# Kernel tuning notes

Hardware: AMD Instinct MI355X
Metric: run time of the kernel (lower is better)

## Reference

```python
import jax, jax.numpy as jnp
import numpy as np

K = 4  # top-k from init
BN_IS_FOLDED = True  # BatchNorm (eval mode) folded into per-channel scale s and shift t


def tconv(x, W):
    # x: (b, C, v, n); W: (Cout, Cin, 3) temporal conv, kernel (3,1,1), padding (1,0,0), no bias
    return jax.lax.conv_general_dilated(
        x, W[:, :, :, None], window_strides=(1, 1),
        padding=((1, 1), (0, 0)), dimension_numbers=('NCHW', 'OIHW', 'NCHW'))


def gcn_single(xn, src, dst, Wg, bg):
    # PyG GCNConv: add self-loops, symmetric normalization, then scatter-add.
    N = xn.shape[0]
    xl = xn @ Wg  # (N, C)
    loop = jnp.arange(N, dtype=src.dtype)
    s = jnp.concatenate([src, loop])
    d = jnp.concatenate([dst, loop])
    deg = jax.ops.segment_sum(jnp.ones(s.shape[0], dtype=xn.dtype), d, num_segments=N)
    dinv = jnp.where(deg > 0, jax.lax.rsqrt(deg), 0.0)
    norm = dinv[s] * dinv[d]
    out = jax.ops.segment_sum(norm[:, None] * xl[s], d, num_segments=N)
    return out + bg


def setup_inputs() -> dict:
    key = jax.random.key(0)
    ks = jax.random.split(key, 10)
    C = 256
    x = jax.random.normal(ks[0], (512, C, 16, 16), dtype=jnp.float32)
    Wd = jax.random.normal(ks[1], (C, C, 3), dtype=jnp.float32) * 0.02
    s1 = 1.0 + 0.1 * jax.random.normal(ks[2], (C,), dtype=jnp.float32)
    t1 = 0.1 * jax.random.normal(ks[3], (C,), dtype=jnp.float32)
    Wg = jax.random.normal(ks[4], (C, C), dtype=jnp.float32) * 0.02
    bg = 0.01 * jax.random.normal(ks[5], (C,), dtype=jnp.float32)
    Wu = jax.random.normal(ks[6], (C, C, 3), dtype=jnp.float32) * 0.02
    s2 = 1.0 + 0.1 * jax.random.normal(ks[7], (C,), dtype=jnp.float32)
    t2 = 0.1 * jax.random.normal(ks[8], (C,), dtype=jnp.float32)
    return {"x": x, "batch": 4, "Wd": Wd, "s1": s1, "t1": t1,
            "Wg": Wg, "bg": bg, "Wu": Wu, "s2": s2, "t2": t2}


def reference(x, batch, Wd, s1, t1, Wg, bg, Wu, s2, t2):
    tlen, c, h, w = x.shape
    b = batch
    v = tlen // b
    hw = h * w
    # (tlen,c,h,w) -> (b,c,v,h*w)
    x4 = x.reshape(b, v, c, h, w).transpose(0, 2, 1, 3, 4).reshape(b, c, v, hw)
    xd = tconv(x4, Wd) * s1[None, :, None, None] + t1[None, :, None, None]  # down_conv + BN(eval)

    # --- dynamic graph build (no-grad in original) ---
    f = jax.lax.stop_gradient(xd).transpose(0, 2, 3, 1)  # (b, v, hw, c)
    f1, f2 = f[:, :-1], f[:, 1:]                          # (b, t_1, hw, c)
    t_1 = v - 1
    sq1 = jnp.sum(f1 * f1, axis=-1)                       # (b,t_1,hw)
    sq2 = jnp.sum(f2 * f2, axis=-1)
    dots = jnp.einsum('btnc,btmc->btnm', f1, f2)
    d2 = jnp.maximum(sq1[..., :, None] + sq2[..., None, :] - 2.0 * dots, 0.0)
    sim = -jnp.sqrt(d2).reshape(b, t_1, hw * hw)
    sim = sim / jnp.maximum(jnp.linalg.norm(sim, axis=-1, keepdims=True), 1e-12)  # F.normalize
    sim = jnp.where(sim < 0.05, 100.0, sim)
    _, idx = jax.lax.top_k(sim, K)                        # (b, t_1, K)
    frame = jnp.arange(t_1, dtype=jnp.int32)[None, :, None]
    row = (idx // hw).astype(jnp.int32) + frame * hw
    col = (idx % hw).astype(jnp.int32) + (frame + 1) * hw
    row = row.reshape(b, -1)
    col = col.reshape(b, -1)
    src = jnp.concatenate([row, col], axis=1)             # forward + reversed edges
    dst = jnp.concatenate([col, row], axis=1)

    # --- per-sample GCN (batched with vmap) ---
    nodes = xd.transpose(0, 2, 3, 1).reshape(b, v * hw, c)  # 'b c v n -> b (v n) c'
    out = jax.vmap(lambda xn, s, d: gcn_single(xn, s, d, Wg, bg))(nodes, src, dst)

    # --- up path ---
    o4 = out.transpose(0, 2, 1).reshape(b, c, v, hw)
    xu = tconv(o4, Wu) * s2[None, :, None, None] + t2[None, :, None, None]
    return xu.reshape(b, c, v, h, w).transpose(0, 2, 1, 3, 4).reshape(tlen, c, h, w)
```

## Files before the change

kernel.cpp:

```cpp
#include <hip/hip_runtime.h>

typedef __attribute__((ext_vector_type(8))) short short8;
typedef __attribute__((ext_vector_type(4))) float f32x4;
typedef unsigned short u16;
typedef unsigned int u32;

__device__ __forceinline__ void gld_lds16(const void* g, void* l) {
  __builtin_amdgcn_global_load_lds((const __attribute__((address_space(1))) void*)g,
                                   (__attribute__((address_space(3))) void*)l,
                                   16, 0, 0);
}

__device__ __forceinline__ u16 f2b(float x) {
  union { float f; u32 u; } v; v.f = x;
  u32 u = v.u;
  return (u16)((u + 0x7FFFu + ((u >> 16) & 1u)) >> 16);
}
__device__ __forceinline__ float b2f(u16 x) {
  union { u32 u; float f; } v; v.u = ((u32)x) << 16; return v.f;
}
__device__ __forceinline__ u32 pack_pair(float lo, float hi) {
  return (u32)f2b(lo) | ((u32)f2b(hi) << 16);
}

__global__ __launch_bounds__(256) void k_prep(const float* __restrict__ Wd, const float* __restrict__ Wg,
                                              const float* __restrict__ Wu,
                                              const float* __restrict__ s1, const float* __restrict__ t1,
                                              const float* __restrict__ bg,
                                              u16* __restrict__ WdT, u16* __restrict__ Wup,
                                              u16* __restrict__ WgS,
                                              float* __restrict__ c0, float* __restrict__ tWg) {
  int blk = blockIdx.x;
  int tid = threadIdx.x;
  if (blk == 1024) {
    int j = tid;
    float a = 0.f;
    for (int co = 0; co < 256; ++co) a += t1[co] * Wg[co * 256 + j];
    tWg[j] = a;
    c0[j] = a + bg[j];
    return;
  }
  int id = blk * 256 + tid;
  if (id < 196608) {
    int kk = id >> 16;
    int rem = id & 65535;
    int a = rem >> 8, b = rem & 255;
    Wup[id] = f2b(Wu[(u32)a * 768 + (u32)b * 3 + kk]);
    WdT[id] = f2b(Wd[(u32)b * 768 + (u32)a * 3 + kk]);
  } else {
    int id2 = id - 196608;
    int j = id2 >> 8, co = id2 & 255;
    WgS[id2] = f2b(Wg[co * 256 + j] * s1[co]);
  }
}

__global__ __launch_bounds__(256) void k_transpose(const float* __restrict__ x, u16* __restrict__ xT) {
  __shared__ u16 tile[64][72];
  int blk = blockIdx.x;
  int tl = blk >> 4;
  int sub = blk & 15;
  int ci0 = (sub >> 2) << 6;
  int p0 = (sub & 3) << 6;
  int tid = threadIdx.x;
  int i = tid >> 2;
  int ch = tid & 3;
  const float* gsrc = x + (size_t)tl * 65536 + (ci0 + i) * 256 + p0 + ch * 16;
  __align__(16) u16 cv[16];
#pragma unroll
  for (int v4 = 0; v4 < 4; ++v4) {
    float4 f = *(const float4*)(gsrc + v4 * 4);
    cv[v4 * 4 + 0] = f2b(f.x);
    cv[v4 * 4 + 1] = f2b(f.y);
    cv[v4 * 4 + 2] = f2b(f.z);
    cv[v4 * 4 + 3] = f2b(f.w);
  }
  *(uint4*)&tile[i][ch * 16] = *(const uint4*)&cv[0];
  *(uint4*)&tile[i][ch * 16 + 8] = *(const uint4*)&cv[8];
  __syncthreads();
  __align__(16) u16 tmp[16];
#pragma unroll
  for (int cc = 0; cc < 16; ++cc) tmp[cc] = tile[ch * 16 + cc][i];
  u16* gdst = xT + (size_t)tl * 65536 + (p0 + i) * 256 + ci0 + ch * 16;
  *(uint4*)(gdst) = *(const uint4*)&tmp[0];
  *(uint4*)(gdst + 8) = *(const uint4*)&tmp[8];
}

__device__ __forceinline__ void stage_tile(const u16* __restrict__ g, int ldg, u16* s, int w, int lane) {
  int r = lane >> 2;
  int cc = (lane & 3) * 8;
#pragma unroll
  for (int j = 0; j < 2; ++j) {
    gld_lds16(g + (w * 32 + j * 16 + r) * ldg + cc, s + (w * 32 + j * 16) * 32);
  }
}

__device__ __forceinline__ void mfma_tiles(const u16* sA, const u16* sB, f32x4 acc[4][4],
                                           int wr, int wc, int lane) {
  int m16 = lane & 15;
  int q8 = (lane >> 4) * 8;
  short8 a[4], b[4];
#pragma unroll
  for (int mi = 0; mi < 4; ++mi) a[mi] = *(const short8*)(sA + (wr * 64 + mi * 16 + m16) * 32 + q8);
#pragma unroll
  for (int ni = 0; ni < 4; ++ni) b[ni] = *(const short8*)(sB + (wc * 64 + ni * 16 + m16) * 32 + q8);
#pragma unroll
  for (int mi = 0; mi < 4; ++mi)
#pragma unroll
    for (int ni = 0; ni < 4; ++ni)
      acc[mi][ni] = __builtin_amdgcn_mfma_f32_16x16x32_bf16(a[mi], b[ni], acc[mi][ni], 0, 0, 0);
}

__device__ __forceinline__ void store_pairs(u16* base, int row0, int stride, int colb,
                                            const float v[4], bool ev) {
  float pv[4];
#pragma unroll
  for (int r = 0; r < 4; ++r) pv[r] = __shfl_xor(v[r], 1, 64);
  u32 wd0 = ev ? pack_pair(v[0], pv[0]) : pack_pair(pv[0], v[0]);
  u32 wd1 = ev ? pack_pair(v[1], pv[1]) : pack_pair(pv[1], v[1]);
  u32 wd2 = ev ? pack_pair(v[2], pv[2]) : pack_pair(pv[2], v[2]);
  u32 wd3 = ev ? pack_pair(v[3], pv[3]) : pack_pair(pv[3], v[3]);
  u32 wa = ev ? wd0 : wd2;
  u32 wb = ev ? wd1 : wd3;
  int rs = ev ? 0 : 2;
  *(u32*)(base + (size_t)(row0 + rs) * stride + colb) = wa;
  *(u32*)(base + (size_t)(row0 + rs + 1) * stride + colb) = wb;
}

__device__ __forceinline__ void store_pairs_f32(float* base, int row0, int stride, int colb,
                                                const float v[4], bool ev) {
  float pv[4];
#pragma unroll
  for (int r = 0; r < 4; ++r) pv[r] = __shfl_xor(v[r], 1, 64);
  float2 wa, wb;
  if (ev) { wa = make_float2(v[0], pv[0]); wb = make_float2(v[1], pv[1]); }
  else    { wa = make_float2(pv[2], v[2]); wb = make_float2(pv[3], v[3]); }
  int rs = ev ? 0 : 2;
  *(float2*)(base + (size_t)(row0 + rs) * stride + colb) = wa;
  *(float2*)(base + (size_t)(row0 + rs + 1) * stride + colb) = wb;
}

__global__ __launch_bounds__(256) void k_wcomb(const u16* __restrict__ WgS, const u16* __restrict__ WdT,
                                               u16* __restrict__ Wcomb) {
  __shared__ u16 sA[128 * 32];
  __shared__ u16 sB[128 * 32];
  int blk = blockIdx.x;
  int kk = blk >> 2;
  int tile = blk & 3;
  int tm = tile >> 1, tn = tile & 1;
  int tid = threadIdx.x, lane = tid & 63, w = tid >> 6;
  int wr = w >> 1, wc = w & 1;
  f32x4 acc[4][4];
#pragma unroll
  for (int i = 0; i < 4; ++i)
#pragma unroll
    for (int j = 0; j < 4; ++j) acc[i][j] = (f32x4){0.f, 0.f, 0.f, 0.f};
  const u16* gA = WgS + (size_t)(tm * 128) * 256;
  const u16* gB = WdT + (size_t)kk * 65536 + (size_t)(tn * 128) * 256;
  for (int ks = 0; ks < 8; ++ks) {
    stage_tile(gA + ks * 32, 256, sA, w, lane);
    stage_tile(gB + ks * 32, 256, sB, w, lane);
    __syncthreads();
    mfma_tiles(sA, sB, acc, wr, wc, lane);
    __syncthreads();
  }
  int q = lane >> 4, c = lane & 15;
  bool ev = (lane & 1) == 0;
  u16* obase = Wcomb + (size_t)kk * 65536;
#pragma unroll
  for (int mi = 0; mi < 4; ++mi) {
    int row0 = tm * 128 + wr * 64 + mi * 16 + q * 4;
#pragma unroll
    for (int ni = 0; ni < 4; ++ni) {
      float v[4];
#pragma unroll
      for (int r = 0; r < 4; ++r) v[r] = acc[mi][ni][r];
      int colb = tn * 128 + wc * 64 + ni * 16 + (c & ~1);
      store_pairs(obase, row0, 256, colb, v, ev);
    }
  }
}

__global__ __launch_bounds__(256) void k_g12(const u16* __restrict__ xT, const u16* __restrict__ Wcomb,
                                             const float* __restrict__ c0, const float* __restrict__ tWg,
                                             u16* __restrict__ outp, float* __restrict__ edge) {
  __shared__ u16 sA[2][128 * 32];
  __shared__ u16 sB[2][128 * 32];
  int b = blockIdx.x;
  int logical = (b & 7) * 256 + (b >> 3);
  int bt = logical >> 2;
  int tile = logical & 3;
  int tm = tile >> 1, tn = tile & 1;
  int t = bt & 127;
  int tid = threadIdx.x, lane = tid & 63, w = tid >> 6;
  int wr = w >> 1, wc = w & 1;
  f32x4 acc[4][4];
#pragma unroll
  for (int i = 0; i < 4; ++i)
#pragma unroll
    for (int j = 0; j < 4; ++j) acc[i][j] = (f32x4){0.f, 0.f, 0.f, 0.f};

  const u16* Ap[3];
  const u16* Bp[3];
  int nf = 0;
#pragma unroll
  for (int kk = 0; kk < 3; ++kk) {
    int tp = t - 1 + kk;
    if (tp < 0 || tp > 127) continue;
    Ap[nf] = xT + ((size_t)(bt - t + tp) * 256 + tm * 128) * 256;
    Bp[nf] = Wcomb + (size_t)kk * 65536 + (size_t)(tn * 128) * 256;
    ++nf;
  }
  int nc = nf * 8;
  stage_tile(Ap[0], 256, sA[0], w, lane);
  stage_tile(Bp[0], 256, sB[0], w, lane);
  __syncthreads();
  for (int c = 0; c < nc; ++c) {
    int nx = c + 1;
    if (nx < nc) {
      stage_tile(Ap[nx >> 3] + (nx & 7) * 32, 256, sA[nx & 1], w, lane);
      stage_tile(Bp[nx >> 3] + (nx & 7) * 32, 256, sB[nx & 1], w, lane);
    }
    mfma_tiles(sA[c & 1], sB[c & 1], acc, wr, wc, lane);
    __syncthreads();
  }

  int q = lane >> 4, cc16 = lane & 15;
  bool ev = (lane & 1) == 0;
  float c0v[4], tWgv[4];
#pragma unroll
  for (int ni = 0; ni < 4; ++ni) {
    int j = tn * 128 + wc * 64 + ni * 16 + cc16;
    c0v[ni] = c0[j];
    tWgv[ni] = tWg[j];
  }
  bool eblk = (tm == 0) && (wr == 0) && (q == 0);
  u16* obase = outp + (size_t)bt * 65536;
#pragma unroll
  for (int mi = 0; mi < 4; ++mi) {
    int row0 = tm * 128 + wr * 64 + mi * 16 + q * 4;
#pragma unroll
    for (int ni = 0; ni < 4; ++ni) {
      float v[4];
#pragma unroll
      for (int r = 0; r < 4; ++r) v[r] = acc[mi][ni][r] + c0v[ni];
      int colb = tn * 128 + wc * 64 + ni * 16 + (cc16 & ~1);
      store_pairs(obase, row0, 256, colb, v, ev);
      if (eblk && mi == 0) {
        float vE[4];
#pragma unroll
        for (int r = 0; r < 4; ++r) vE[r] = acc[0][ni][r] + tWgv[ni];
        store_pairs_f32(edge + (size_t)bt * 1024, 0, 256, colb, vE, ev);
      }
    }
  }
}

__device__ __forceinline__ float dinv0(int t) {
  if (t == 0) return 0.44721359549995793f;
  if (t == 127) return 0.7071067811865476f;
  return 0.4082482904638631f;
}
__global__ __launch_bounds__(256) void k_fix(const float* __restrict__ edge, const float* __restrict__ bg,
                                             u16* __restrict__ outp) {
  int bt = blockIdx.x;
  int t = bt & 127;
  int j = threadIdx.x;
  const float ISQ2 = 0.7071067811865476f;
  float bgv = bg[j];
  float e_t = edge[(size_t)bt * 1024 + j];
  float At = dinv0(t);
  float o0 = bgv + At * At * e_t;
  if (t <= 126) {
    float At1 = dinv0(t + 1);
    const float* en = edge + (size_t)(bt + 1) * 1024;
    float s = At1 * en[j] + ISQ2 * (en[256 + j] + en[512 + j] + en[768 + j]);
    o0 += At * s;
  }
  float em1 = 0.f, Atm1 = 0.f;
  if (t >= 1) {
    Atm1 = dinv0(t - 1);
    em1 = edge[(size_t)(bt - 1) * 1024 + j];
    o0 += At * Atm1 * em1;
  }
  u16* ob = outp + (size_t)bt * 65536;
  ob[j] = f2b(o0);
#pragma unroll
  for (int k = 1; k <= 3; ++k) {
    float m = edge[(size_t)bt * 1024 + k * 256 + j];
    float ok = (t == 0) ? (bgv + m) : (bgv + 0.5f * m + ISQ2 * Atm1 * em1);
    ob[k * 256 + j] = f2b(ok);
  }
}

__global__ __launch_bounds__(256) void k_g3(const u16* __restrict__ outp, const u16* __restrict__ Wup,
                                            const float* __restrict__ s2, const float* __restrict__ t2,
                                            float* __restrict__ y) {
  __shared__ u16 sA[2][128 * 32];
  __shared__ u16 sB[2][128 * 32];
  __shared__ float ss2[128], st2[128];
  int b = blockIdx.x;
  int logical = (b & 7) * 256 + (b >> 3);
  int bt = logical >> 2;
  int tile = logical & 3;
  int tm = tile >> 1, tn = tile & 1;
  int t = bt & 127;
  int tid = threadIdx.x, lane = tid & 63, w = tid >> 6;
  int wr = w >> 1, wc = w & 1;
  if (tid < 128) {
    int co = tm * 128 + tid;
    ss2[tid] = s2[co];
    st2[tid] = t2[co];
  }
  f32x4 acc[4][4];
#pragma unroll
  for (int i = 0; i < 4; ++i)
#pragma unroll
    for (int j = 0; j < 4; ++j) acc[i][j] = (f32x4){0.f, 0.f, 0.f, 0.f};

  const u16* Ap[3];
  const u16* Bp[3];
  int nf = 0;
#pragma unroll
  for (int kk = 0; kk < 3; ++kk) {
    int tp = t - 1 + kk;
    if (tp < 0 || tp > 127) continue;
    Ap[nf] = Wup + (size_t)kk * 65536 + (size_t)(tm * 128) * 256;
    Bp[nf] = outp + ((size_t)(bt - t + tp) * 256 + tn * 128) * 256;
    ++nf;
  }
  int nc = nf * 8;
  stage_tile(Ap[0], 256, sA[0], w, lane);
  stage_tile(Bp[0], 256, sB[0], w, lane);
  __syncthreads();
  for (int c = 0; c < nc; ++c) {
    int nx = c + 1;
    if (nx < nc) {
      stage_tile(Ap[nx >> 3] + (nx & 7) * 32, 256, sA[nx & 1], w, lane);
      stage_tile(Bp[nx >> 3] + (nx & 7) * 32, 256, sB[nx & 1], w, lane);
    }
    mfma_tiles(sA[c & 1], sB[c & 1], acc, wr, wc, lane);
    __syncthreads();
  }

  int q = lane >> 4, cc16 = lane & 15;
  bool ev = (lane & 1) == 0;
  float* ybase = y + (size_t)bt * 65536;
#pragma unroll
  for (int mi = 0; mi < 4; ++mi) {
    int rl = wr * 64 + mi * 16 + q * 4;
    float sv[4], tv[4];
#pragma unroll
    for (int r = 0; r < 4; ++r) { sv[r] = ss2[rl + r]; tv[r] = st2[rl + r]; }
#pragma unroll
    for (int ni = 0; ni < 4; ++ni) {
      float v[4];
#pragma unroll
      for (int r = 0; r < 4; ++r) v[r] = acc[mi][ni][r] * sv[r] + tv[r];
      int colb = tn * 128 + wc * 64 + ni * 16 + (cc16 & ~1);
      store_pairs_f32(ybase, tm * 128 + rl, 256, colb, v, ev);
    }
  }
}

extern "C" void kernel_launch(void* const* d_in, const int* in_sizes, int n_in,
                              void* d_out, int out_size, void* d_ws, size_t ws_size,
                              hipStream_t stream) {
  (void)in_sizes; (void)n_in; (void)out_size; (void)ws_size;
  const float* x  = (const float*)d_in[0];
  const float* Wd = (const float*)d_in[2];
  const float* s1 = (const float*)d_in[3];
  const float* t1 = (const float*)d_in[4];
  const float* Wg = (const float*)d_in[5];
  const float* bg = (const float*)d_in[6];
  const float* Wu = (const float*)d_in[7];
  const float* s2 = (const float*)d_in[8];
  const float* t2 = (const float*)d_in[9];
  float* y = (float*)d_out;
  char* ws = (char*)d_ws;
  u16*   outp  = (u16*)(ws);
  u16*   xT    = (u16*)(ws + 67108864);
  float* edge  = (float*)(ws + 134217728);
  u16*   WdT   = (u16*)(ws + 134217728);
  u16*   WgS   = (u16*)(ws + 134611072);
  u16*   Wup   = (u16*)(ws + 136314880);
  u16*   Wcomb = (u16*)(ws + 136708096);
  float* c0    = (float*)(ws + 137101312);
  float* tWg   = (float*)(ws + 137102336);

  k_prep<<<dim3(1025), dim3(256), 0, stream>>>(Wd, Wg, Wu, s1, t1, bg, WdT, Wup, WgS, c0, tWg);
  k_wcomb<<<dim3(12), dim3(256), 0, stream>>>(WgS, WdT, Wcomb);
  k_transpose<<<dim3(8192), dim3(256), 0, stream>>>(x, xT);
  k_g12<<<dim3(2048), dim3(256), 0, stream>>>(xT, Wcomb, c0, tWg, outp, edge);
  k_fix<<<dim3(512), dim3(256), 0, stream>>>(edge, bg, outp);
  k_g3<<<dim3(2048), dim3(256), 0, stream>>>(outp, Wup, s2, t2, y);
}
```

Baseline: 431.1 us.

## Use 256x256 tiles with zero-padded frames and 8-wave pipelined MFMA GEMM core

Restructures both GEMM kernels to have each 512-thread block compute a full 256x256 output tile per frame. Boundary frames are zero-padded on either side, so the three temporal taps always make a uniform K=768 loop with no branching. The new core uses XOR-swizzled LDS layout, finer-grained staging interleaved with MFMA quads, s_setprio and explicit vmcnt waits. The edge buffer is moved into the output array as scratch. This trades extra zeroing work and MFMA on padded zero frames for larger data reuse and better overlap of loads with compute.

```diff
diff --git a/kernel.cpp b/kernel.cpp
--- a/kernel.cpp
+++ b/kernel.cpp
@@ -4,6 +4,8 @@
 typedef __attribute__((ext_vector_type(4))) float f32x4;
 typedef unsigned short u16;
 typedef unsigned int u32;
+
+#define FENCE() asm volatile("" ::: "memory")
 
 __device__ __forceinline__ void gld_lds16(const void* g, void* l) {
   __builtin_amdgcn_global_load_lds((const __attribute__((address_space(1))) void*)g,
@@ -54,7 +56,18 @@
   }
 }
 
-__global__ __launch_bounds__(256) void k_transpose(const float* __restrict__ x, u16* __restrict__ xT) {
+__global__ __launch_bounds__(256) void k_zero(u16* __restrict__ outz, u16* __restrict__ xTz) {
+  int gid = blockIdx.x * 256 + threadIdx.x;
+  int i = gid * 8;
+  int buf = (i >= 327680) ? 1 : 0;
+  int wi = i - buf * 327680;
+  int f = wi >> 16;
+  int off = wi & 65535;
+  u16* dst = (buf ? xTz : outz) + (size_t)f * 129 * 65536 + off;
+  *(uint4*)dst = make_uint4(0u, 0u, 0u, 0u);
+}
+
+__global__ __launch_bounds__(256) void k_transpose(const float* __restrict__ x, u16* __restrict__ xTz) {
   __shared__ u16 tile[64][72];
   int blk = blockIdx.x;
   int tl = blk >> 4;
@@ -80,7 +93,8 @@
   __align__(16) u16 tmp[16];
 #pragma unroll
   for (int cc = 0; cc < 16; ++cc) tmp[cc] = tile[ch * 16 + cc][i];
-  u16* gdst = xT + (size_t)tl * 65536 + (p0 + i) * 256 + ci0 + ch * 16;
+  int fi = (tl >> 7) * 129 + (tl & 127) + 1;
+  u16* gdst = xTz + (size_t)fi * 65536 + (p0 + i) * 256 + ci0 + ch * 16;
   *(uint4*)(gdst) = *(const uint4*)&tmp[0];
   *(uint4*)(gdst + 8) = *(const uint4*)&tmp[8];
 }
@@ -180,77 +194,176 @@
   }
 }
 
-__global__ __launch_bounds__(256) void k_g12(const u16* __restrict__ xT, const u16* __restrict__ Wcomb,
-                                             const float* __restrict__ c0, const float* __restrict__ tWg,
-                                             u16* __restrict__ outp, float* __restrict__ edge) {
-  __shared__ u16 sA[2][128 * 32];
-  __shared__ u16 sB[2][128 * 32];
-  int b = blockIdx.x;
-  int logical = (b & 7) * 256 + (b >> 3);
-  int bt = logical >> 2;
-  int tile = logical & 3;
-  int tm = tile >> 1, tn = tile & 1;
-  int t = bt & 127;
-  int tid = threadIdx.x, lane = tid & 63, w = tid >> 6;
-  int wr = w >> 1, wc = w & 1;
-  f32x4 acc[4][4];
-#pragma unroll
-  for (int i = 0; i < 4; ++i)
+
+__device__ __forceinline__ void stage_part(int s, const u16* Ab, const u16* Bb,
+                                           u16* sA, u16* sB, int wuni, int g0) {
+  if (s >= 48) return;
+  const int tau = s >> 2;
+  const int pt = s & 3;
+  const int toff = ((tau >> 2) << 16) + ((tau & 3) << 6);
+  const int half = pt & 1;
+  const u16* src = ((pt & 2) ? Ab : Bb) + toff + (half << 15) + g0;
+  u16* dst = ((pt & 2) ? sA : sB) + ((tau & 1) << 14) + (half << 13) + wuni;
+  gld_lds16(src, dst);
+  gld_lds16(src + 16384, dst + 4096);
+}
+
+template<int QUAD, int NH>
+__device__ __forceinline__ void mfma_quad(f32x4 (&acc)[8][4], const short8 (&af)[2][4],
+                                          const short8 (&bf)[2][2][2]) {
+#pragma unroll
+  for (int k = 0; k < 2; ++k)
+#pragma unroll
+    for (int m = 0; m < 4; ++m)
+#pragma unroll
+      for (int nj = 0; nj < 2; ++nj)
+        acc[QUAD * 4 + m][NH * 2 + nj] = __builtin_amdgcn_mfma_f32_16x16x32_bf16(
+            af[k][m], bf[NH][k][nj], acc[QUAD * 4 + m][NH * 2 + nj], 0, 0, 0);
+}
+
+__device__ __forceinline__ void gemm256_core(const u16* __restrict__ Ab, const u16* __restrict__ Bb,
+                                             u16* sA, u16* sB, int tid, f32x4 (&acc)[8][4]) {
+  const int lane = tid & 63;
+  const int w = tid >> 6;
+  const int wr = w >> 2;
+  const int wc = w & 3;
+  const int m16 = lane & 15;
+  const int xorm = (lane & 7) << 4;
+  const int q16b = (lane >> 4) << 4;
+  const int koffe0 = ((q16b) ^ xorm) >> 1;
+  const int koffe1 = ((64 + q16b) ^ xorm) >> 1;
+  const int srow = tid >> 3;
+  const int scol = ((tid & 7) ^ (srow & 7)) << 3;
+  const int g0 = srow * 256 + scol;
+  const int wuni = w << 9;
+
+#pragma unroll
+  for (int i = 0; i < 8; ++i)
 #pragma unroll
     for (int j = 0; j < 4; ++j) acc[i][j] = (f32x4){0.f, 0.f, 0.f, 0.f};
 
-  const u16* Ap[3];
-  const u16* Bp[3];
-  int nf = 0;
-#pragma unroll
-  for (int kk = 0; kk < 3; ++kk) {
-    int tp = t - 1 + kk;
-    if (tp < 0 || tp > 127) continue;
-    Ap[nf] = xT + ((size_t)(bt - t + tp) * 256 + tm * 128) * 256;
-    Bp[nf] = Wcomb + (size_t)kk * 65536 + (size_t)(tn * 128) * 256;
-    ++nf;
-  }
-  int nc = nf * 8;
-  stage_tile(Ap[0], 256, sA[0], w, lane);
-  stage_tile(Bp[0], 256, sB[0], w, lane);
-  __syncthreads();
-  for (int c = 0; c < nc; ++c) {
-    int nx = c + 1;
-    if (nx < nc) {
-      stage_tile(Ap[nx >> 3] + (nx & 7) * 32, 256, sA[nx & 1], w, lane);
-      stage_tile(Bp[nx >> 3] + (nx & 7) * 32, 256, sB[nx & 1], w, lane);
-    }
-    mfma_tiles(sA[c & 1], sB[c & 1], acc, wr, wc, lane);
-    __syncthreads();
-  }
-
+#pragma unroll
+  for (int s = 0; s < 7; ++s) stage_part(s, Ab, Bb, sA, sB, wuni, g0);
+  asm volatile("s_waitcnt vmcnt(6)" ::: "memory");
+  __builtin_amdgcn_s_barrier();
+  FENCE();
+
+  short8 af[2][4];
+  short8 bf[2][2][2];
+#pragma unroll 2
+  for (int kt = 0; kt < 12; ++kt) {
+    const int cb = kt & 1;
+    const u16* aH = sA + cb * 16384 + wr * 8192;
+    const u16* bH = sB + cb * 16384 + (wc >> 1) * 8192;
+    const int bR0 = (wc & 1) << 6;
+#pragma unroll
+    for (int m = 0; m < 4; ++m) {
+      const u16* p = aH + (m * 16 + m16) * 64;
+      af[0][m] = *(const short8*)(p + koffe0);
+      af[1][m] = *(const short8*)(p + koffe1);
+    }
+#pragma unroll
+    for (int nh = 0; nh < 2; ++nh)
+#pragma unroll
+      for (int nj = 0; nj < 2; ++nj) {
+        const u16* p = bH + (bR0 + (nh * 2 + nj) * 16 + m16) * 64;
+        bf[nh][0][nj] = *(const short8*)(p + koffe0);
+        bf[nh][1][nj] = *(const short8*)(p + koffe1);
+      }
+    stage_part(4 * kt + 7, Ab, Bb, sA, sB, wuni, g0);
+    FENCE();
+    __builtin_amdgcn_s_barrier();
+    FENCE();
+    __builtin_amdgcn_s_setprio(1);
+    mfma_quad<0, 0>(acc, af, bf);
+    __builtin_amdgcn_s_setprio(0);
+    FENCE();
+    __builtin_amdgcn_s_barrier();
+    FENCE();
+    stage_part(4 * kt + 8, Ab, Bb, sA, sB, wuni, g0);
+    FENCE();
+    __builtin_amdgcn_s_barrier();
+    FENCE();
+    __builtin_amdgcn_s_setprio(1);
+    mfma_quad<0, 1>(acc, af, bf);
+    __builtin_amdgcn_s_setprio(0);
+    FENCE();
+    __builtin_amdgcn_s_barrier();
+    FENCE();
+#pragma unroll
+    for (int m = 0; m < 4; ++m) {
+      const u16* p = aH + (64 + m * 16 + m16) * 64;
+      af[0][m] = *(const short8*)(p + koffe0);
+      af[1][m] = *(const short8*)(p + koffe1);
+    }
+    stage_part(4 * kt + 9, Ab, Bb, sA, sB, wuni, g0);
+    FENCE();
+    __builtin_amdgcn_s_barrier();
+    FENCE();
+    __builtin_amdgcn_s_setprio(1);
+    mfma_quad<1, 0>(acc, af, bf);
+    __builtin_amdgcn_s_setprio(0);
+    FENCE();
+    __builtin_amdgcn_s_barrier();
+    FENCE();
+    stage_part(4 * kt + 10, Ab, Bb, sA, sB, wuni, g0);
+    FENCE();
+    __builtin_amdgcn_s_barrier();
+    FENCE();
+    __builtin_amdgcn_s_setprio(1);
+    mfma_quad<1, 1>(acc, af, bf);
+    __builtin_amdgcn_s_setprio(0);
+    if (kt < 10) asm volatile("s_waitcnt vmcnt(6)" ::: "memory");
+    else         asm volatile("s_waitcnt vmcnt(0)" ::: "memory");
+    __builtin_amdgcn_s_barrier();
+    FENCE();
+  }
+}
+
+__global__ __launch_bounds__(512, 2) void k_g12(const u16* __restrict__ xTz, const u16* __restrict__ Wcomb,
+                                                const float* __restrict__ c0, const float* __restrict__ tWg,
+                                                u16* __restrict__ outz, float* __restrict__ edge) {
+  __shared__ u16 sA[32768];
+  __shared__ u16 sB[32768];
+  int bsw = (int)blockIdx.x;
+  int bt = (bsw & 7) * 64 + (bsw >> 3);
+  int b = bt >> 7, t = bt & 127;
+  int tid = threadIdx.x;
+  const u16* Ab = xTz + (size_t)(b * 129 + t) * 65536;
+  const u16* Bb = Wcomb;
+  f32x4 acc[8][4];
+  gemm256_core(Ab, Bb, sA, sB, tid, acc);
+
+  int lane = tid & 63, w = tid >> 6, wr = w >> 2, wc = w & 3;
   int q = lane >> 4, cc16 = lane & 15;
   bool ev = (lane & 1) == 0;
   float c0v[4], tWgv[4];
 #pragma unroll
   for (int ni = 0; ni < 4; ++ni) {
-    int j = tn * 128 + wc * 64 + ni * 16 + cc16;
+    int j = wc * 64 + ni * 16 + cc16;
     c0v[ni] = c0[j];
     tWgv[ni] = tWg[j];
   }
-  bool eblk = (tm == 0) && (wr == 0) && (q == 0);
-  u16* obase = outp + (size_t)bt * 65536;
-#pragma unroll
-  for (int mi = 0; mi < 4; ++mi) {
-    int row0 = tm * 128 + wr * 64 + mi * 16 + q * 4;
+  u16* obase = outz + (size_t)(b * 129 + t + 1) * 65536;
+#pragma unroll
+  for (int mi = 0; mi < 8; ++mi) {
+    int row0 = wr * 128 + mi * 16 + q * 4;
 #pragma unroll
     for (int ni = 0; ni < 4; ++ni) {
       float v[4];
 #pragma unroll
       for (int r = 0; r < 4; ++r) v[r] = acc[mi][ni][r] + c0v[ni];
-      int colb = tn * 128 + wc * 64 + ni * 16 + (cc16 & ~1);
-      store_pairs(obase, row0, 256, colb, v, ev);
-      if (eblk && mi == 0) {
-        float vE[4];
-#pragma unroll
-        for (int r = 0; r < 4; ++r) vE[r] = acc[0][ni][r] + tWgv[ni];
-        store_pairs_f32(edge + (size_t)bt * 1024, 0, 256, colb, vE, ev);
-      }
+      store_pairs(obase, row0, 256, wc * 64 + ni * 16 + (cc16 & ~1), v, ev);
+    }
+  }
+  if (wr == 0 && q == 0) {
+    float* eb = edge + (size_t)bt * 1024;
+#pragma unroll
+    for (int ni = 0; ni < 4; ++ni) {
+      float vE[4];
+#pragma unroll
+      for (int r = 0; r < 4; ++r) vE[r] = acc[0][ni][r] + tWgv[ni];
+      store_pairs_f32(eb, 0, 256, wc * 64 + ni * 16 + (cc16 & ~1), vE, ev);
     }
   }
 }
@@ -261,8 +374,9 @@
   return 0.4082482904638631f;
 }
 __global__ __launch_bounds__(256) void k_fix(const float* __restrict__ edge, const float* __restrict__ bg,
-                                             u16* __restrict__ outp) {
+                                             u16* __restrict__ outz) {
   int bt = blockIdx.x;
+  int b = bt >> 7;
   int t = bt & 127;
   int j = threadIdx.x;
   const float ISQ2 = 0.7071067811865476f;
@@ -282,7 +396,7 @@
     em1 = edge[(size_t)(bt - 1) * 1024 + j];
     o0 += At * Atm1 * em1;
   }
-  u16* ob = outp + (size_t)bt * 65536;
+  u16* ob = outz + (size_t)(b * 129 + t + 1) * 65536;
   ob[j] = f2b(o0);
 #pragma unroll
   for (int k = 1; k <= 3; ++k) {
@@ -292,72 +406,37 @@
   }
 }
 
-__global__ __launch_bounds__(256) void k_g3(const u16* __restrict__ outp, const u16* __restrict__ Wup,
-                                            const float* __restrict__ s2, const float* __restrict__ t2,
-                                            float* __restrict__ y) {
-  __shared__ u16 sA[2][128 * 32];
-  __shared__ u16 sB[2][128 * 32];
-  __shared__ float ss2[128], st2[128];
-  int b = blockIdx.x;
-  int logical = (b & 7) * 256 + (b >> 3);
-  int bt = logical >> 2;
-  int tile = logical & 3;
-  int tm = tile >> 1, tn = tile & 1;
-  int t = bt & 127;
-  int tid = threadIdx.x, lane = tid & 63, w = tid >> 6;
-  int wr = w >> 1, wc = w & 1;
-  if (tid < 128) {
-    int co = tm * 128 + tid;
-    ss2[tid] = s2[co];
-    st2[tid] = t2[co];
-  }
-  f32x4 acc[4][4];
-#pragma unroll
-  for (int i = 0; i < 4; ++i)
-#pragma unroll
-    for (int j = 0; j < 4; ++j) acc[i][j] = (f32x4){0.f, 0.f, 0.f, 0.f};
-
-  const u16* Ap[3];
-  const u16* Bp[3];
-  int nf = 0;
-#pragma unroll
-  for (int kk = 0; kk < 3; ++kk) {
-    int tp = t - 1 + kk;
-    if (tp < 0 || tp > 127) continue;
-    Ap[nf] = Wup + (size_t)kk * 65536 + (size_t)(tm * 128) * 256;
-    Bp[nf] = outp + ((size_t)(bt - t + tp) * 256 + tn * 128) * 256;
-    ++nf;
-  }
-  int nc = nf * 8;
-  stage_tile(Ap[0], 256, sA[0], w, lane);
-  stage_tile(Bp[0], 256, sB[0], w, lane);
-  __syncthreads();
-  for (int c = 0; c < nc; ++c) {
-    int nx = c + 1;
-    if (nx < nc) {
-      stage_tile(Ap[nx >> 3] + (nx & 7) * 32, 256, sA[nx & 1], w, lane);
-      stage_tile(Bp[nx >> 3] + (nx & 7) * 32, 256, sB[nx & 1], w, lane);
-    }
-    mfma_tiles(sA[c & 1], sB[c & 1], acc, wr, wc, lane);
-    __syncthreads();
-  }
-
+__global__ __launch_bounds__(512, 2) void k_g3(const u16* __restrict__ outz, const u16* __restrict__ Wup,
+                                               const float* __restrict__ s2, const float* __restrict__ t2,
+                                               float* __restrict__ y) {
+  __shared__ u16 sA[32768];
+  __shared__ u16 sB[32768];
+  int bsw = (int)blockIdx.x;
+  int bt = (bsw & 7) * 64 + (bsw >> 3);
+  int b = bt >> 7, t = bt & 127;
+  int tid = threadIdx.x;
+  const u16* Ab = Wup;
+  const u16* Bb = outz + (size_t)(b * 129 + t) * 65536;
+  f32x4 acc[8][4];
+  gemm256_core(Ab, Bb, sA, sB, tid, acc);
+
+  int lane = tid & 63, w = tid >> 6, wr = w >> 2, wc = w & 3;
   int q = lane >> 4, cc16 = lane & 15;
   bool ev = (lane & 1) == 0;
   float* ybase = y + (size_t)bt * 65536;
 #pragma unroll
-  for (int mi = 0; mi < 4; ++mi) {
-    int rl = wr * 64 + mi * 16 + q * 4;
-    float sv[4], tv[4];
-#pragma unroll
-    for (int r = 0; r < 4; ++r) { sv[r] = ss2[rl + r]; tv[r] = st2[rl + r]; }
+  for (int mi = 0; mi < 8; ++mi) {
+    int rl = wr * 128 + mi * 16 + q * 4;
+    float4 s4 = *(const float4*)(s2 + rl);
+    float4 t4 = *(const float4*)(t2 + rl);
 #pragma unroll
     for (int ni = 0; ni < 4; ++ni) {
       float v[4];
-#pragma unroll
-      for (int r = 0; r < 4; ++r) v[r] = acc[mi][ni][r] * sv[r] + tv[r];
-      int colb = tn * 128 + wc * 64 + ni * 16 + (cc16 & ~1);
-      store_pairs_f32(ybase, tm * 128 + rl, 256, colb, v, ev);
+      v[0] = acc[mi][ni][0] * s4.x + t4.x;
+      v[1] = acc[mi][ni][1] * s4.y + t4.y;
+      v[2] = acc[mi][ni][2] * s4.z + t4.z;
+      v[3] = acc[mi][ni][3] * s4.w + t4.w;
+      store_pairs_f32(ybase, rl, 256, wc * 64 + ni * 16 + (cc16 & ~1), v, ev);
     }
   }
 }
@@ -377,20 +456,21 @@
   const float* t2 = (const float*)d_in[9];
   float* y = (float*)d_out;
   char* ws = (char*)d_ws;
-  u16*   outp  = (u16*)(ws);
-  u16*   xT    = (u16*)(ws + 67108864);
-  float* edge  = (float*)(ws + 134217728);
-  u16*   WdT   = (u16*)(ws + 134217728);
-  u16*   WgS   = (u16*)(ws + 134611072);
-  u16*   Wup   = (u16*)(ws + 136314880);
-  u16*   Wcomb = (u16*)(ws + 136708096);
-  float* c0    = (float*)(ws + 137101312);
-  float* tWg   = (float*)(ws + 137102336);
+  u16*   outz  = (u16*)(ws);
+  u16*   xTz   = (u16*)(ws + 67764224);
+  u16*   WdT   = (u16*)(ws + 135528448);
+  u16*   WgS   = (u16*)(ws + 135921664);
+  u16*   Wup   = (u16*)(ws + 136052736);
+  u16*   Wcomb = (u16*)(ws + 136445952);
+  float* c0    = (float*)(ws + 136839168);
+  float* tWg   = (float*)(ws + 136840192);
+  float* edge  = (float*)d_out;
 
   k_prep<<<dim3(1025), dim3(256), 0, stream>>>(Wd, Wg, Wu, s1, t1, bg, WdT, Wup, WgS, c0, tWg);
   k_wcomb<<<dim3(12), dim3(256), 0, stream>>>(WgS, WdT, Wcomb);
-  k_transpose<<<dim3(8192), dim3(256), 0, stream>>>(x, xT);
-  k_g12<<<dim3(2048), dim3(256), 0, stream>>>(xT, Wcomb, c0, tWg, outp, edge);
-  k_fix<<<dim3(512), dim3(256), 0, stream>>>(edge, bg, outp);
-  k_g3<<<dim3(2048), dim3(256), 0, stream>>>(outp, Wup, s2, t2, y);
-}
+  k_zero<<<dim3(320), dim3(256), 0, stream>>>(outz, xTz);
+  k_transpose<<<dim3(8192), dim3(256), 0, stream>>>(x, xTz);
+  k_g12<<<dim3(512), dim3(512), 0, stream>>>(xTz, Wcomb, c0, tWg, outz, edge);
+  k_fix<<<dim3(512), dim3(256), 0, stream>>>(edge, bg, outz);
+  k_g3<<<dim3(512), dim3(512), 0, stream>>>(outz, Wup, s2, t2, y);
+}
```

New measurement: 398.4 us. 7.6% less time.
